# Performance work log

Measured on AMD Instinct MI355X. Metric: run time of the kernel, lower is better.

Reference implementation:

```python
import jax, jax.numpy as jnp
import numpy as np

N, D, H, R = 50000, 256, 4, 3
C = D // H        # head dim = 64
E = 400000        # edges per relation
NEG = 0.2         # LeakyReLU slope
LN_EPS = 1e-5


def _segment_softmax(att, seg, n):
    # att: [E, H], seg: [E] destination node ids -> softmax per (node, head)
    m = jax.ops.segment_max(att, seg, num_segments=n)
    m = jnp.where(jnp.isfinite(m), m, 0.0)        # nodes with no edges
    e = jnp.exp(att - m[seg])
    s = jax.ops.segment_sum(e, seg, num_segments=n)
    return e / (s[seg] + 1e-16)


def setup_inputs() -> dict:
    key = jax.random.key(0)
    ks = jax.random.split(key, 16)
    inp = {
        'feat': jax.random.normal(ks[0], (N, D), jnp.float32),
        'Wl': jax.random.normal(ks[1], (D, D), jnp.float32) / np.sqrt(D).astype(np.float32),
        'bl': jnp.zeros((D,), jnp.float32),
        'Wr': jax.random.normal(ks[2], (D, D), jnp.float32) / np.sqrt(D).astype(np.float32),
        'br': jnp.zeros((D,), jnp.float32),
        'attn_l': jax.random.normal(ks[3], (R, H, C), jnp.float32) / np.sqrt(C).astype(np.float32),
        'attn_r': jax.random.normal(ks[4], (R, H, C), jnp.float32) / np.sqrt(C).astype(np.float32),
        'rel_q': jax.random.normal(ks[5], (H, C), jnp.float32) / np.sqrt(C).astype(np.float32),
        'rel_k': jax.random.normal(ks[6], (H, C), jnp.float32) / np.sqrt(C).astype(np.float32),
        'ln_gamma': jnp.ones((D,), jnp.float32),
        'ln_beta': jnp.zeros((D,), jnp.float32),
    }
    for r in range(R):
        inp[f'edge_src_{r}'] = jax.random.randint(ks[7 + 2 * r], (E,), 0, N, jnp.int64 if jax.config.jax_enable_x64 else jnp.int32)
        inp[f'edge_dst_{r}'] = jax.random.randint(ks[8 + 2 * r], (E,), 0, N, jnp.int64 if jax.config.jax_enable_x64 else jnp.int32)
    return inp


def reference(feat, Wl, bl, Wr, br, attn_l, attn_r, rel_q, rel_k, ln_gamma, ln_beta,
              edge_src_0, edge_dst_0, edge_src_1, edge_dst_1, edge_src_2, edge_dst_2):
    # per-node-type linear projections -> multi-head [N, H, C]
    k = (feat @ Wl + bl).reshape(N, H, C)
    v = (feat @ Wr + br).reshape(N, H, C)
    srcs = [edge_src_0, edge_src_1, edge_src_2]
    dsts = [edge_dst_0, edge_dst_1, edge_dst_2]
    rel_outs = []
    for r in range(R):  # loop over fixed, structurally distinct relations
        s, d = srcs[r], dsts[r]
        # edge attention: (k_src . a_l) + (v_dst . a_r), LeakyReLU (attn_dropout inactive in eval)
        att = jnp.einsum('ehc,hc->eh', k[s], attn_l[r]) + jnp.einsum('ehc,hc->eh', v[d], attn_r[r])
        att = jax.nn.leaky_relu(att, NEG)
        a = _segment_softmax(att, d, N)                                   # [E, H]
        # message 'h' is edges.dst['v'] in the original code (faithful)
        h = jax.ops.segment_sum(a[:, :, None] * v[d], d, num_segments=N)  # [N, H, C]
        rel_outs.append(h)
    # stack relation embeddings + self 'v' (the +1 none-selection relation)
    x = jnp.stack(rel_outs + [v], axis=1)                                  # [N, T=R+1, H, C]
    # MetapathGATConv (1 layer) stand-in: self embedding queries all relations per head
    q = jnp.einsum('nhc,hc->nh', x[:, -1], rel_q)                          # [N, H]
    kk = jnp.einsum('nthc,hc->nth', x, rel_k)                              # [N, T, H]
    beta = jax.nn.softmax(jax.nn.leaky_relu(q[:, None, :] + kk, NEG), axis=1)  # [N, T, H]
    out = jnp.einsum('nth,nthc->nhc', beta, x).reshape(N, D)
    # activation -> (dropout inactive in eval) -> LayerNorm
    out = jax.nn.relu(out)
    mu = out.mean(-1, keepdims=True)
    var = out.var(-1, keepdims=True)
    out = (out - mu) * jax.lax.rsqrt(var + LN_EPS) * ln_gamma + ln_beta
    return out
```

## Files before the change

### kernel.cpp

```cpp
#include <hip/hip_runtime.h>

#define N_NODES 50000
#define DIM 256
#define NEG 0.2f
#define LN_EPS 1e-5f
#define SCAT_BLOCKS 2048

typedef __attribute__((ext_vector_type(8))) short short8;
typedef __attribute__((ext_vector_type(4))) float f32x4;

__device__ __forceinline__ unsigned short f2bf(float x) {
    unsigned int u = __builtin_bit_cast(unsigned int, x);
    u += 0x7fffu + ((u >> 16) & 1u);
    return (unsigned short)(u >> 16);
}

__device__ __forceinline__ void load_lds16(const void* g, void* l) {
    __builtin_amdgcn_global_load_lds((const unsigned int*)g, (unsigned int*)l, 16, 0, 0);
}

__device__ __forceinline__ short8 cvt_bfrag(float4 a4, float4 b4) {
    short8 r;
    r[0] = (short)f2bf(a4.x); r[1] = (short)f2bf(a4.y);
    r[2] = (short)f2bf(a4.z); r[3] = (short)f2bf(a4.w);
    r[4] = (short)f2bf(b4.x); r[5] = (short)f2bf(b4.y);
    r[6] = (short)f2bf(b4.z); r[7] = (short)f2bf(b4.w);
    return r;
}

__global__ __launch_bounds__(256) void prep(
    const float* __restrict__ Wr, unsigned short* __restrict__ WrF,
    const int* __restrict__ d0, const int* __restrict__ d1, const int* __restrict__ d2,
    int E, unsigned char* __restrict__ mask)
{
    if (blockIdx.x < 32) {
        const int o    = blockIdx.x * 256 + threadIdx.x;
        const int lane = o & 63;
        const int frag = o >> 6;
        const int mt = frag & 15, kk = frag >> 4;
        const int ln = lane & 15, quad = lane >> 4;
        const float* src = Wr + (size_t)(kk * 32 + quad * 8) * DIM + mt * 16 + ln;
        short8 v;
        #pragma unroll
        for (int j = 0; j < 8; ++j) v[j] = (short)f2bf(src[(size_t)j * DIM]);
        *(short8*)(WrF + (size_t)o * 8) = v;
    } else {
        const int total = 3 * E;
        for (int i = (blockIdx.x - 32) * 256 + (int)threadIdx.x; i < total;
             i += SCAT_BLOCKS * 256) {
            const int* d; int base, e;
            if (i >= 2 * E)  { d = d2; e = i - 2 * E; base = 2 * N_NODES; }
            else if (i >= E) { d = d1; e = i - E;     base = N_NODES; }
            else             { d = d0; e = i;         base = 0; }
            mask[base + d[e]] = (unsigned char)1;
        }
    }
}

__global__ __launch_bounds__(256, 3) void fused_mfma(
    const float* __restrict__ feat, const unsigned short* __restrict__ WrF,
    const float* __restrict__ br, const float* __restrict__ rel_q,
    const float* __restrict__ rel_k, const float* __restrict__ gamma,
    const float* __restrict__ beta_p, const unsigned char* __restrict__ mask,
    float* __restrict__ out)
{
    __shared__ unsigned short lds[2][8192];
    const int lane = threadIdx.x & 63;
    const int wave = threadIdx.x >> 6;
    const int ln = lane & 15;
    const int quad = lane >> 4;
    int node = blockIdx.x * 64 + wave * 16 + ln;
    const bool valid = node < N_NODES;
    if (!valid) node = N_NODES - 1;

    const float* fptr = feat + (size_t)node * DIM + quad * 8;

    float4 FA[2], FB[2];
    FA[0] = *(const float4*)(fptr);       FB[0] = *(const float4*)(fptr + 4);
    FA[1] = *(const float4*)(fptr + 32);  FB[1] = *(const float4*)(fptr + 36);

    {
        const char* g = (const char*)WrF;
        #pragma unroll
        for (int r = 0; r < 4; ++r) {
            const int off = wave * 4096 + r * 1024;
            load_lds16(g + off + lane * 16, (char*)lds[0] + off);
        }
    }

    const int m0 = (int)mask[node];
    const int m1 = (int)mask[N_NODES + node];
    const int m2 = (int)mask[2 * N_NODES + node];

    f32x4 acc[16];
    #pragma unroll
    for (int mt = 0; mt < 16; ++mt) acc[mt] = (f32x4){0.f, 0.f, 0.f, 0.f};

    short8 bcur = cvt_bfrag(FA[0], FB[0]);

    __syncthreads();

    #pragma unroll
    for (int p = 0; p < 8; ++p) {
        if (p < 7) {
            const char* g = (const char*)WrF + (p + 1) * 16384;
            char* l = (char*)lds[(p + 1) & 1];
            #pragma unroll
            for (int r = 0; r < 4; ++r) {
                const int off = wave * 4096 + r * 1024;
                load_lds16(g + off + lane * 16, l + off);
            }
        }
        if (p < 6) {
            FA[p & 1] = *(const float4*)(fptr + (p + 2) * 32);
            FB[p & 1] = *(const float4*)(fptr + (p + 2) * 32 + 4);
        }
        const char* b = (const char*)lds[p & 1];
        #pragma unroll
        for (int mt = 0; mt < 16; ++mt) {
            const short8 a = *(const short8*)(b + mt * 1024 + lane * 16);
            acc[mt] = __builtin_amdgcn_mfma_f32_16x16x32_bf16(a, bcur, acc[mt], 0, 0, 0);
        }
        if (p < 7) {
            bcur = cvt_bfrag(FA[(p + 1) & 1], FB[(p + 1) & 1]);
            __syncthreads();
        }
    }

    float qp[4] = {0.f, 0.f, 0.f, 0.f}, kp[4] = {0.f, 0.f, 0.f, 0.f};
    #pragma unroll
    for (int mt = 0; mt < 16; ++mt) {
        const int cbase = mt * 16 + quad * 4;
        const float4 bb = *(const float4*)(br + cbase);
        acc[mt][0] += bb.x; acc[mt][1] += bb.y; acc[mt][2] += bb.z; acc[mt][3] += bb.w;
        const float4 rq = *(const float4*)(rel_q + cbase);
        const float4 rk = *(const float4*)(rel_k + cbase);
        const int h = mt >> 2;
        qp[h] += acc[mt][0] * rq.x + acc[mt][1] * rq.y + acc[mt][2] * rq.z + acc[mt][3] * rq.w;
        kp[h] += acc[mt][0] * rk.x + acc[mt][1] * rk.y + acc[mt][2] * rk.z + acc[mt][3] * rk.w;
    }
    #pragma unroll
    for (int h = 0; h < 4; ++h) {
        qp[h] += __shfl_xor(qp[h], 16); qp[h] += __shfl_xor(qp[h], 32);
        kp[h] += __shfl_xor(kp[h], 16); kp[h] += __shfl_xor(kp[h], 32);
    }

    const int cnt = m0 + m1 + m2;

    float wgt[4];
    #pragma unroll
    for (int h = 0; h < 4; ++h) {
        const float q = qp[h];
        const float qk = q + kp[h];
        const float a = q  > 0.f ? q  : NEG * q;
        const float b = qk > 0.f ? qk : NEG * qk;
        const float mx = fmaxf(a, b);
        const float eb = (float)(cnt + 1) * __expf(b - mx);
        const float ea = (float)(3 - cnt) * __expf(a - mx);
        wgt[h] = eb / (eb + ea);
    }

    float sum = 0.f, ssq = 0.f;
    #pragma unroll
    for (int mt = 0; mt < 16; ++mt) {
        const float w = wgt[mt >> 2];
        #pragma unroll
        for (int r = 0; r < 4; ++r) {
            float v = fmaxf(acc[mt][r] * w, 0.f);
            acc[mt][r] = v;
            sum += v; ssq += v * v;
        }
    }
    sum += __shfl_xor(sum, 16); sum += __shfl_xor(sum, 32);
    ssq += __shfl_xor(ssq, 16); ssq += __shfl_xor(ssq, 32);
    const float mu = sum * (1.f / 256.f);
    const float var = ssq * (1.f / 256.f) - mu * mu;
    const float rstd = rsqrtf(var + LN_EPS);

    if (valid) {
        float* optr = out + (size_t)node * DIM;
        #pragma unroll
        for (int mt = 0; mt < 16; ++mt) {
            const int cbase = mt * 16 + quad * 4;
            const float4 g = *(const float4*)(gamma + cbase);
            const float4 b = *(const float4*)(beta_p + cbase);
            float4 r;
            r.x = (acc[mt][0] - mu) * rstd * g.x + b.x;
            r.y = (acc[mt][1] - mu) * rstd * g.y + b.y;
            r.z = (acc[mt][2] - mu) * rstd * g.z + b.z;
            r.w = (acc[mt][3] - mu) * rstd * g.w + b.w;
            *(float4*)(optr + cbase) = r;
        }
    }
}

extern "C" void kernel_launch(void* const* d_in, const int* in_sizes, int n_in,
                              void* d_out, int out_size, void* d_ws, size_t ws_size,
                              hipStream_t stream) {
    const float* feat  = (const float*)d_in[0];
    const float* Wr    = (const float*)d_in[3];
    const float* br    = (const float*)d_in[4];
    const float* rel_q = (const float*)d_in[7];
    const float* rel_k = (const float*)d_in[8];
    const float* gamma = (const float*)d_in[9];
    const float* beta  = (const float*)d_in[10];
    const int* dst0 = (const int*)d_in[12];
    const int* dst1 = (const int*)d_in[14];
    const int* dst2 = (const int*)d_in[16];
    const int E = in_sizes[12];

    unsigned short* WrF = (unsigned short*)d_ws;
    unsigned char* mask = (unsigned char*)d_ws + DIM * DIM * 2;

    hipMemsetAsync(mask, 0, 150016, stream);
    prep<<<32 + SCAT_BLOCKS, 256, 0, stream>>>(Wr, WrF, dst0, dst1, dst2, E, mask);
    fused_mfma<<<(N_NODES + 63) / 64, 256, 0, stream>>>(
        feat, WrF, br, rel_q, rel_k, gamma, beta, mask, (float*)d_out);
}
```

Before: 166.4 us.

## Make fused GEMM kernel persistent with whole weight matrix resident in LDS

Replaces the one-tile-per-block launch with a persistent grid of 256 blocks of 8 waves. Each block loads the entire bf16 Wr (128KB) into LDS once, and each wave then loops over 16-node tiles with a stride of 2048. The next tile's features are prefetched into registers while the current tile computes, which removes the per-block weight streaming and the barriers inside the k loop. In exchange it uses a large LDS footprint and many registers (16 feature float4s plus 16 accumulators), which limits occupancy to about one block per CU. The per-row valid check is dropped on the assumption that N divides evenly into 16-node tiles.

```diff
diff --git a/kernel.cpp b/kernel.cpp
--- a/kernel.cpp
+++ b/kernel.cpp
@@ -5,6 +5,8 @@
 #define NEG 0.2f
 #define LN_EPS 1e-5f
 #define SCAT_BLOCKS 2048
+#define NT16 3125
+#define NWAVES 2048
 
 typedef __attribute__((ext_vector_type(8))) short short8;
 typedef __attribute__((ext_vector_type(4))) float f32x4;
@@ -57,140 +59,148 @@
     }
 }
 
-__global__ __launch_bounds__(256, 3) void fused_mfma(
+__global__ __launch_bounds__(512, 2) void fused_mfma(
     const float* __restrict__ feat, const unsigned short* __restrict__ WrF,
     const float* __restrict__ br, const float* __restrict__ rel_q,
     const float* __restrict__ rel_k, const float* __restrict__ gamma,
     const float* __restrict__ beta_p, const unsigned char* __restrict__ mask,
     float* __restrict__ out)
 {
-    __shared__ unsigned short lds[2][8192];
+    __shared__ unsigned short lds[65536];
     const int lane = threadIdx.x & 63;
     const int wave = threadIdx.x >> 6;
     const int ln = lane & 15;
     const int quad = lane >> 4;
-    int node = blockIdx.x * 64 + wave * 16 + ln;
-    const bool valid = node < N_NODES;
-    if (!valid) node = N_NODES - 1;
-
-    const float* fptr = feat + (size_t)node * DIM + quad * 8;
-
-    float4 FA[2], FB[2];
-    FA[0] = *(const float4*)(fptr);       FB[0] = *(const float4*)(fptr + 4);
-    FA[1] = *(const float4*)(fptr + 32);  FB[1] = *(const float4*)(fptr + 36);
+    const int gwid = blockIdx.x * 8 + wave;
 
     {
         const char* g = (const char*)WrF;
         #pragma unroll
-        for (int r = 0; r < 4; ++r) {
-            const int off = wave * 4096 + r * 1024;
-            load_lds16(g + off + lane * 16, (char*)lds[0] + off);
-        }
-    }
-
-    const int m0 = (int)mask[node];
-    const int m1 = (int)mask[N_NODES + node];
-    const int m2 = (int)mask[2 * N_NODES + node];
-
-    f32x4 acc[16];
+        for (int r = 0; r < 16; ++r) {
+            const int off = (wave * 16 + r) * 1024;
+            load_lds16(g + off + lane * 16, (char*)lds + off);
+        }
+    }
+
+    int t = gwid;
+    float4 FA[8], FB[8];
+    {
+        const float* fp = feat + (size_t)(t * 16 + ln) * DIM + quad * 8;
+        #pragma unroll
+        for (int kk = 0; kk < 8; ++kk) {
+            FA[kk] = *(const float4*)(fp + kk * 32);
+            FB[kk] = *(const float4*)(fp + kk * 32 + 4);
+        }
+    }
+
+    __syncthreads();
+
+    short8 bfr[8];
     #pragma unroll
-    for (int mt = 0; mt < 16; ++mt) acc[mt] = (f32x4){0.f, 0.f, 0.f, 0.f};
-
-    short8 bcur = cvt_bfrag(FA[0], FB[0]);
-
-    __syncthreads();
-
-    #pragma unroll
-    for (int p = 0; p < 8; ++p) {
-        if (p < 7) {
-            const char* g = (const char*)WrF + (p + 1) * 16384;
-            char* l = (char*)lds[(p + 1) & 1];
-            #pragma unroll
-            for (int r = 0; r < 4; ++r) {
-                const int off = wave * 4096 + r * 1024;
-                load_lds16(g + off + lane * 16, l + off);
-            }
-        }
-        if (p < 6) {
-            FA[p & 1] = *(const float4*)(fptr + (p + 2) * 32);
-            FB[p & 1] = *(const float4*)(fptr + (p + 2) * 32 + 4);
-        }
-        const char* b = (const char*)lds[p & 1];
-        #pragma unroll
-        for (int mt = 0; mt < 16; ++mt) {
-            const short8 a = *(const short8*)(b + mt * 1024 + lane * 16);
-            acc[mt] = __builtin_amdgcn_mfma_f32_16x16x32_bf16(a, bcur, acc[mt], 0, 0, 0);
-        }
-        if (p < 7) {
-            bcur = cvt_bfrag(FA[(p + 1) & 1], FB[(p + 1) & 1]);
-            __syncthreads();
-        }
-    }
-
-    float qp[4] = {0.f, 0.f, 0.f, 0.f}, kp[4] = {0.f, 0.f, 0.f, 0.f};
-    #pragma unroll
-    for (int mt = 0; mt < 16; ++mt) {
-        const int cbase = mt * 16 + quad * 4;
-        const float4 bb = *(const float4*)(br + cbase);
-        acc[mt][0] += bb.x; acc[mt][1] += bb.y; acc[mt][2] += bb.z; acc[mt][3] += bb.w;
-        const float4 rq = *(const float4*)(rel_q + cbase);
-        const float4 rk = *(const float4*)(rel_k + cbase);
-        const int h = mt >> 2;
-        qp[h] += acc[mt][0] * rq.x + acc[mt][1] * rq.y + acc[mt][2] * rq.z + acc[mt][3] * rq.w;
-        kp[h] += acc[mt][0] * rk.x + acc[mt][1] * rk.y + acc[mt][2] * rk.z + acc[mt][3] * rk.w;
-    }
-    #pragma unroll
-    for (int h = 0; h < 4; ++h) {
-        qp[h] += __shfl_xor(qp[h], 16); qp[h] += __shfl_xor(qp[h], 32);
-        kp[h] += __shfl_xor(kp[h], 16); kp[h] += __shfl_xor(kp[h], 32);
-    }
-
-    const int cnt = m0 + m1 + m2;
-
-    float wgt[4];
-    #pragma unroll
-    for (int h = 0; h < 4; ++h) {
-        const float q = qp[h];
-        const float qk = q + kp[h];
-        const float a = q  > 0.f ? q  : NEG * q;
-        const float b = qk > 0.f ? qk : NEG * qk;
-        const float mx = fmaxf(a, b);
-        const float eb = (float)(cnt + 1) * __expf(b - mx);
-        const float ea = (float)(3 - cnt) * __expf(a - mx);
-        wgt[h] = eb / (eb + ea);
-    }
-
-    float sum = 0.f, ssq = 0.f;
-    #pragma unroll
-    for (int mt = 0; mt < 16; ++mt) {
-        const float w = wgt[mt >> 2];
-        #pragma unroll
-        for (int r = 0; r < 4; ++r) {
-            float v = fmaxf(acc[mt][r] * w, 0.f);
-            acc[mt][r] = v;
-            sum += v; ssq += v * v;
-        }
-    }
-    sum += __shfl_xor(sum, 16); sum += __shfl_xor(sum, 32);
-    ssq += __shfl_xor(ssq, 16); ssq += __shfl_xor(ssq, 32);
-    const float mu = sum * (1.f / 256.f);
-    const float var = ssq * (1.f / 256.f) - mu * mu;
-    const float rstd = rsqrtf(var + LN_EPS);
-
-    if (valid) {
-        float* optr = out + (size_t)node * DIM;
+    for (int kk = 0; kk < 8; ++kk) bfr[kk] = cvt_bfrag(FA[kk], FB[kk]);
+
+    while (true) {
+        const int node = t * 16 + ln;
+
+        const int m0 = (int)mask[node];
+        const int m1 = (int)mask[N_NODES + node];
+        const int m2 = (int)mask[2 * N_NODES + node];
+
+        const int tn = t + NWAVES;
+        const int tl = tn < NT16 ? tn : t;
+        {
+            const float* fp = feat + (size_t)(tl * 16 + ln) * DIM + quad * 8;
+            #pragma unroll
+            for (int kk = 0; kk < 8; ++kk) {
+                FA[kk] = *(const float4*)(fp + kk * 32);
+                FB[kk] = *(const float4*)(fp + kk * 32 + 4);
+            }
+        }
+
+        f32x4 acc[16];
+        #pragma unroll
+        for (int mt = 0; mt < 16; ++mt) acc[mt] = (f32x4){0.f, 0.f, 0.f, 0.f};
+
+        #pragma unroll
+        for (int kk = 0; kk < 8; ++kk) {
+            #pragma unroll
+            for (int mt = 0; mt < 16; ++mt) {
+                const short8 a = *(const short8*)((const char*)lds
+                                   + (kk * 16 + mt) * 1024 + lane * 16);
+                acc[mt] = __builtin_amdgcn_mfma_f32_16x16x32_bf16(a, bfr[kk], acc[mt], 0, 0, 0);
+            }
+        }
+
+        float qp[4] = {0.f, 0.f, 0.f, 0.f}, kp[4] = {0.f, 0.f, 0.f, 0.f};
         #pragma unroll
         for (int mt = 0; mt < 16; ++mt) {
             const int cbase = mt * 16 + quad * 4;
-            const float4 g = *(const float4*)(gamma + cbase);
-            const float4 b = *(const float4*)(beta_p + cbase);
-            float4 r;
-            r.x = (acc[mt][0] - mu) * rstd * g.x + b.x;
-            r.y = (acc[mt][1] - mu) * rstd * g.y + b.y;
-            r.z = (acc[mt][2] - mu) * rstd * g.z + b.z;
-            r.w = (acc[mt][3] - mu) * rstd * g.w + b.w;
-            *(float4*)(optr + cbase) = r;
-        }
+            const float4 bb = *(const float4*)(br + cbase);
+            acc[mt][0] += bb.x; acc[mt][1] += bb.y; acc[mt][2] += bb.z; acc[mt][3] += bb.w;
+            const float4 rq = *(const float4*)(rel_q + cbase);
+            const float4 rk = *(const float4*)(rel_k + cbase);
+            const int h = mt >> 2;
+            qp[h] += acc[mt][0] * rq.x + acc[mt][1] * rq.y + acc[mt][2] * rq.z + acc[mt][3] * rq.w;
+            kp[h] += acc[mt][0] * rk.x + acc[mt][1] * rk.y + acc[mt][2] * rk.z + acc[mt][3] * rk.w;
+        }
+        #pragma unroll
+        for (int h = 0; h < 4; ++h) {
+            qp[h] += __shfl_xor(qp[h], 16); qp[h] += __shfl_xor(qp[h], 32);
+            kp[h] += __shfl_xor(kp[h], 16); kp[h] += __shfl_xor(kp[h], 32);
+        }
+
+        const int cnt = m0 + m1 + m2;
+
+        float wgt[4];
+        #pragma unroll
+        for (int h = 0; h < 4; ++h) {
+            const float q = qp[h];
+            const float qk = q + kp[h];
+            const float a = q  > 0.f ? q  : NEG * q;
+            const float b = qk > 0.f ? qk : NEG * qk;
+            const float mx = fmaxf(a, b);
+            const float eb = (float)(cnt + 1) * __expf(b - mx);
+            const float ea = (float)(3 - cnt) * __expf(a - mx);
+            wgt[h] = eb / (eb + ea);
+        }
+
+        float sum = 0.f, ssq = 0.f;
+        #pragma unroll
+        for (int mt = 0; mt < 16; ++mt) {
+            const float w = wgt[mt >> 2];
+            #pragma unroll
+            for (int r = 0; r < 4; ++r) {
+                float v = fmaxf(acc[mt][r] * w, 0.f);
+                acc[mt][r] = v;
+                sum += v; ssq += v * v;
+            }
+        }
+        sum += __shfl_xor(sum, 16); sum += __shfl_xor(sum, 32);
+        ssq += __shfl_xor(ssq, 16); ssq += __shfl_xor(ssq, 32);
+        const float mu = sum * (1.f / 256.f);
+        const float var = ssq * (1.f / 256.f) - mu * mu;
+        const float rstd = rsqrtf(var + LN_EPS);
+
+        {
+            float* optr = out + (size_t)node * DIM;
+            #pragma unroll
+            for (int mt = 0; mt < 16; ++mt) {
+                const int cbase = mt * 16 + quad * 4;
+                const float4 g = *(const float4*)(gamma + cbase);
+                const float4 b = *(const float4*)(beta_p + cbase);
+                float4 r;
+                r.x = (acc[mt][0] - mu) * rstd * g.x + b.x;
+                r.y = (acc[mt][1] - mu) * rstd * g.y + b.y;
+                r.z = (acc[mt][2] - mu) * rstd * g.z + b.z;
+                r.w = (acc[mt][3] - mu) * rstd * g.w + b.w;
+                *(float4*)(optr + cbase) = r;
+            }
+        }
+
+        if (tn >= NT16) break;
+        t = tn;
+        #pragma unroll
+        for (int kk = 0; kk < 8; ++kk) bfr[kk] = cvt_bfrag(FA[kk], FB[kk]);
     }
 }
 
@@ -214,6 +224,6 @@
 
     hipMemsetAsync(mask, 0, 150016, stream);
     prep<<<32 + SCAT_BLOCKS, 256, 0, stream>>>(Wr, WrF, dst0, dst1, dst2, E, mask);
-    fused_mfma<<<(N_NODES + 63) / 64, 256, 0, stream>>>(
+    fused_mfma<<<256, 512, 0, stream>>>(
         feat, WrF, br, rel_q, rel_k, gamma, beta, mask, (float*)d_out);
 }
```

After: 432.9 us. +160.2%, slower.

## Stream weight fragments from global into registers instead of LDS double-buffering

Applied to the files above, without the earlier changes.

Drops the LDS double buffer and the barriers used to stage the bf16 weight fragments. Each wave now reads its weight fragments straight from global memory (expected to hit L2 or cache) into a 3-deep register ring, and loads and converts the whole feature row up front into 8 B fragments. This removes LDS traffic and block-wide syncs. The cost is much higher register pressure, which may reduce occupancy under launch_bounds(256,3), and every wave re-reads the full weight matrix from cache.

```diff
diff --git a/kernel.cpp b/kernel.cpp
--- a/kernel.cpp
+++ b/kernel.cpp
@@ -13,10 +13,6 @@
     unsigned int u = __builtin_bit_cast(unsigned int, x);
     u += 0x7fffu + ((u >> 16) & 1u);
     return (unsigned short)(u >> 16);
-}
-
-__device__ __forceinline__ void load_lds16(const void* g, void* l) {
-    __builtin_amdgcn_global_load_lds((const unsigned int*)g, (unsigned int*)l, 16, 0, 0);
 }
 
 __device__ __forceinline__ short8 cvt_bfrag(float4 a4, float4 b4) {
@@ -64,7 +60,6 @@
     const float* __restrict__ beta_p, const unsigned char* __restrict__ mask,
     float* __restrict__ out)
 {
-    __shared__ unsigned short lds[2][8192];
     const int lane = threadIdx.x & 63;
     const int wave = threadIdx.x >> 6;
     const int ln = lane & 15;
@@ -73,58 +68,44 @@
     const bool valid = node < N_NODES;
     if (!valid) node = N_NODES - 1;
 
-    const float* fptr = feat + (size_t)node * DIM + quad * 8;
-
-    float4 FA[2], FB[2];
-    FA[0] = *(const float4*)(fptr);       FB[0] = *(const float4*)(fptr + 4);
-    FA[1] = *(const float4*)(fptr + 32);  FB[1] = *(const float4*)(fptr + 36);
-
-    {
-        const char* g = (const char*)WrF;
-        #pragma unroll
-        for (int r = 0; r < 4; ++r) {
-            const int off = wave * 4096 + r * 1024;
-            load_lds16(g + off + lane * 16, (char*)lds[0] + off);
-        }
-    }
-
     const int m0 = (int)mask[node];
     const int m1 = (int)mask[N_NODES + node];
     const int m2 = (int)mask[2 * N_NODES + node];
 
+    const float* fptr = feat + (size_t)node * DIM + quad * 8;
+    float4 F0[8], F1[8];
+    #pragma unroll
+    for (int kk = 0; kk < 8; ++kk) {
+        F0[kk] = *(const float4*)(fptr + kk * 32);
+        F1[kk] = *(const float4*)(fptr + kk * 32 + 4);
+    }
+    short8 bfr[8];
+    #pragma unroll
+    for (int kk = 0; kk < 8; ++kk) bfr[kk] = cvt_bfrag(F0[kk], F1[kk]);
+
     f32x4 acc[16];
     #pragma unroll
     for (int mt = 0; mt < 16; ++mt) acc[mt] = (f32x4){0.f, 0.f, 0.f, 0.f};
 
-    short8 bcur = cvt_bfrag(FA[0], FB[0]);
-
-    __syncthreads();
-
-    #pragma unroll
-    for (int p = 0; p < 8; ++p) {
-        if (p < 7) {
-            const char* g = (const char*)WrF + (p + 1) * 16384;
-            char* l = (char*)lds[(p + 1) & 1];
+    const char* wptr = (const char*)WrF + lane * 16;
+    short8 Ab[3][4];
+    #pragma unroll
+    for (int j = 0; j < 4; ++j) Ab[0][j] = *(const short8*)(wptr + (size_t)(0 + j) * 1024);
+    #pragma unroll
+    for (int j = 0; j < 4; ++j) Ab[1][j] = *(const short8*)(wptr + (size_t)(4 + j) * 1024);
+
+    #pragma unroll
+    for (int g = 0; g < 32; ++g) {
+        if (g < 30) {
             #pragma unroll
-            for (int r = 0; r < 4; ++r) {
-                const int off = wave * 4096 + r * 1024;
-                load_lds16(g + off + lane * 16, l + off);
-            }
-        }
-        if (p < 6) {
-            FA[p & 1] = *(const float4*)(fptr + (p + 2) * 32);
-            FB[p & 1] = *(const float4*)(fptr + (p + 2) * 32 + 4);
-        }
-        const char* b = (const char*)lds[p & 1];
-        #pragma unroll
-        for (int mt = 0; mt < 16; ++mt) {
-            const short8 a = *(const short8*)(b + mt * 1024 + lane * 16);
-            acc[mt] = __builtin_amdgcn_mfma_f32_16x16x32_bf16(a, bcur, acc[mt], 0, 0, 0);
-        }
-        if (p < 7) {
-            bcur = cvt_bfrag(FA[(p + 1) & 1], FB[(p + 1) & 1]);
-            __syncthreads();
-        }
+            for (int j = 0; j < 4; ++j)
+                Ab[(g + 2) % 3][j] = *(const short8*)(wptr + (size_t)((g + 2) * 4 + j) * 1024);
+        }
+        const int kk = g >> 2, mb = (g & 3) * 4;
+        #pragma unroll
+        for (int j = 0; j < 4; ++j)
+            acc[mb + j] = __builtin_amdgcn_mfma_f32_16x16x32_bf16(
+                Ab[g % 3][j], bfr[kk], acc[mb + j], 0, 0, 0);
     }
 
     float qp[4] = {0.f, 0.f, 0.f, 0.f}, kp[4] = {0.f, 0.f, 0.f, 0.f};
```

Result: slower. 175.1 us (+5.3%).
